# Kernel tuning notes

Hardware: AMD Instinct MI355X
Metric: run time of the kernel (lower is better)

Reference implementation:

```python
import jax, jax.numpy as jnp
import numpy as np

B, S, D, E = 4, 4096, 512, 8
H = 4 * D


def setup_inputs() -> dict:
    key = jax.random.key(0)
    ks = jax.random.split(key, 10)
    s_d = 1.0 / np.sqrt(D)
    s_h = 1.0 / np.sqrt(H)
    return {
        "x": jax.random.normal(ks[0], (B, S, D), jnp.float32),
        "Wr": jax.random.uniform(ks[1], (D, E), jnp.float32, -s_d, s_d),
        "br": jax.random.uniform(ks[2], (E,), jnp.float32, -s_d, s_d),
        "Wn": jax.random.uniform(ks[3], (D, E), jnp.float32, -s_d, s_d),
        "bn": jax.random.uniform(ks[4], (E,), jnp.float32, -s_d, s_d),
        "W1": jax.random.uniform(ks[5], (E, D, H), jnp.float32, -s_d, s_d),
        "b1": jax.random.uniform(ks[6], (E, H), jnp.float32, -s_d, s_d),
        "W2": jax.random.uniform(ks[7], (E, H, D), jnp.float32, -s_h, s_h),
        "b2": jax.random.uniform(ks[8], (E, D), jnp.float32, -s_h, s_h),
        "top_k": 2,
    }


def reference(x, Wr, br, Wn, bn, W1, b1, W2, b2, top_k):
    d = x.shape[-1]
    flat = x.reshape(-1, d)                      # [T, D]
    T = flat.shape[0]
    # --- NoisyTopkRouter ---
    logits = flat @ Wr + br                      # [T, E]
    noisy_lin = flat @ Wn + bn                   # [T, E]
    noise = jax.random.normal(jax.random.key(42), logits.shape, logits.dtype)
    noisy_logits = logits + noise * jax.nn.softplus(noisy_lin)
    topv, topi = jax.lax.top_k(noisy_logits, top_k)  # [T, K]
    sparse = jnp.full_like(noisy_logits, -jnp.inf)
    sparse = sparse.at[jnp.arange(T)[:, None], topi].set(topv)
    gate = jax.nn.softmax(sparse, axis=-1)       # zeros at non-topk (exp(-inf)=0)
    # --- expert compute + combine ---
    # gate is exactly 0 for non-selected experts, so dense per-expert compute
    # weighted by gate is math-identical to the masked gather/scatter loop.
    # Dropout(0.1) is identity in eval mode.
    out = jnp.zeros_like(flat)
    n_experts = W1.shape[0]
    for e in range(n_experts):
        h = jax.nn.relu(flat @ W1[e] + b1[e])    # [T, H]
        y = h @ W2[e] + b2[e]                    # [T, D]
        out = out + gate[:, e:e + 1] * y
    return out.reshape(x.shape)
```

## Files before the change

### kernel.cpp

```cpp
#include <hip/hip_runtime.h>
#include <hip/hip_bf16.h>
#include <stdint.h>
#include <math.h>

#define T_TOKENS 16384
#define DIM      512
#define NEXP     8
#define HID      2048

typedef __attribute__((ext_vector_type(8))) __bf16 bf16x8;
typedef __attribute__((ext_vector_type(16))) float f32x16;

__device__ __forceinline__ f32x16 mfma32(bf16x8 a, bf16x8 b, f32x16 c) {
  return __builtin_amdgcn_mfma_f32_32x32x16_bf16(a, b, c, 0, 0, 0);
}

__device__ __forceinline__ void glds16(const __bf16* g, __bf16* l) {
  __builtin_amdgcn_global_load_lds((const __attribute__((address_space(1))) void*)g,
                                   (__attribute__((address_space(3))) void*)l, 16, 0, 0);
}

#define WAITVM(n) asm volatile("s_waitcnt vmcnt(" #n ")" ::: "memory")
#define WAITLGKM0 asm volatile("s_waitcnt lgkmcnt(0)" ::: "memory")
#define SBAR      asm volatile("s_barrier" ::: "memory")
#define SCHEDB    __builtin_amdgcn_sched_barrier(0)
#define ADV3(v)   v = ((v) == 2) ? 0 : ((v) + 1)

__device__ __forceinline__ void threefry2x32(uint32_t k0, uint32_t k1,
                                             uint32_t x0, uint32_t x1,
                                             uint32_t* o0, uint32_t* o1) {
  uint32_t ks0 = k0, ks1 = k1, ks2 = k0 ^ k1 ^ 0x1BD11BDAu;
#define TF_ROT(v, d) (((v) << (d)) | ((v) >> (32 - (d))))
#define TF_ROUND(r) { x0 += x1; x1 = TF_ROT(x1, r); x1 ^= x0; }
  x0 += ks0; x1 += ks1;
  TF_ROUND(13) TF_ROUND(15) TF_ROUND(26) TF_ROUND(6)
  x0 += ks1; x1 += ks2 + 1u;
  TF_ROUND(17) TF_ROUND(29) TF_ROUND(16) TF_ROUND(24)
  x0 += ks2; x1 += ks0 + 2u;
  TF_ROUND(13) TF_ROUND(15) TF_ROUND(26) TF_ROUND(6)
  x0 += ks0; x1 += ks1 + 3u;
  TF_ROUND(17) TF_ROUND(29) TF_ROUND(16) TF_ROUND(24)
  x0 += ks1; x1 += ks2 + 4u;
  TF_ROUND(13) TF_ROUND(15) TF_ROUND(26) TF_ROUND(6)
  x0 += ks2; x1 += ks0 + 5u;
#undef TF_ROUND
#undef TF_ROT
  *o0 = x0; *o1 = x1;
}

__device__ __forceinline__ float erfinv_xla(float x) {
  float w = -log1pf(__fmul_rn(-x, x));
  float p;
  if (w < 5.0f) {
    w = __fadd_rn(w, -2.5f);
    p = 2.81022636e-08f;
    p = __fadd_rn(3.43273939e-07f, __fmul_rn(p, w));
    p = __fadd_rn(-3.5233877e-06f, __fmul_rn(p, w));
    p = __fadd_rn(-4.39150654e-06f, __fmul_rn(p, w));
    p = __fadd_rn(0.00021858087f, __fmul_rn(p, w));
    p = __fadd_rn(-0.00125372503f, __fmul_rn(p, w));
    p = __fadd_rn(-0.00417768164f, __fmul_rn(p, w));
    p = __fadd_rn(0.246640727f, __fmul_rn(p, w));
    p = __fadd_rn(1.50140941f, __fmul_rn(p, w));
  } else {
    w = __fadd_rn(sqrtf(w), -3.0f);
    p = -0.000200214257f;
    p = __fadd_rn(0.000100950558f, __fmul_rn(p, w));
    p = __fadd_rn(0.00134934322f, __fmul_rn(p, w));
    p = __fadd_rn(-0.00367342844f, __fmul_rn(p, w));
    p = __fadd_rn(0.00573950773f, __fmul_rn(p, w));
    p = __fadd_rn(-0.0076224613f, __fmul_rn(p, w));
    p = __fadd_rn(0.00943887047f, __fmul_rn(p, w));
    p = __fadd_rn(1.00167406f, __fmul_rn(p, w));
    p = __fadd_rn(2.83297682f, __fmul_rn(p, w));
  }
  return __fmul_rn(p, x);
}

__device__ __forceinline__ float jax_normal_at(uint32_t i) {
  uint32_t o0, o1;
  threefry2x32(0u, 42u, 0u, i, &o0, &o1);
  uint32_t bits = o0 ^ o1;
  float f = __fadd_rn(__uint_as_float((bits >> 9) | 0x3f800000u), -1.0f);
  const float lo = -0.99999994f;
  float u = fmaxf(lo, __fadd_rn(__fmul_rn(f, 2.0f), lo));
  return __fmul_rn(1.4142135623730951f, erfinv_xla(u));
}

__global__ __launch_bounds__(256) void prep_router(
    const float* __restrict__ x, const float* __restrict__ Wr, const float* __restrict__ br,
    const float* __restrict__ Wn, const float* __restrict__ bn,
    const float* __restrict__ W1, const float* __restrict__ W2,
    __bf16* __restrict__ W1p, __bf16* __restrict__ W2p,
    uint8_t* __restrict__ fillRow, uint32_t* __restrict__ ltok2,
    float* __restrict__ out) {
  __shared__ float Ls[64][68];
  __shared__ float WrS[4224], WnS[4224];
  __shared__ int lhist[8];
  const int tid = threadIdx.x;
  const int blk = blockIdx.x;

  {
    float4 z = {0.f, 0.f, 0.f, 0.f};
    ((float4*)out)[blk * 512 + tid] = z;
    ((float4*)out)[blk * 512 + 256 + tid] = z;
  }

  {
    const float* src; __bf16* dst; int R, C, e, rt, ct;
    if (blk < 2048) { e = blk >> 8; int rem = blk & 255; rt = rem >> 5; ct = rem & 31;
                      src = W1; dst = W1p; R = 512; C = 2048; }
    else            { int v2 = blk - 2048; e = v2 >> 8; int rem = v2 & 255; rt = rem >> 3; ct = rem & 7;
                      src = W2; dst = W2p; R = 2048; C = 512; }
    const float* sp = src + (size_t)e * R * C + (size_t)(rt * 64) * C + ct * 64;
    int row = tid >> 4, col = (tid & 15) * 4;
#pragma unroll
    for (int it = 0; it < 4; ++it)
      *(float4*)&Ls[it * 16 + row][col] = *(const float4*)(sp + (size_t)(it * 16 + row) * C + col);
    __syncthreads();
    int KO = R >> 3;
#pragma unroll
    for (int q = 0; q < 2; ++q) {
      int f = tid + q * 256;
      int lc = f & 31, kol = (f >> 5) & 7, ntl = f >> 8;
      bf16x8 vv;
#pragma unroll
      for (int j = 0; j < 8; ++j) vv[j] = (__bf16)Ls[kol * 8 + j][ntl * 32 + lc];
      size_t idx = ((size_t)(e * (C >> 5) + ct * 2 + ntl) * KO + rt * 8 + kol) * 256 + lc * 8;
      *(bf16x8*)(dst + idx) = vv;
    }
  }

  if (blk >= 256) return;

#pragma unroll
  for (int i = 0; i < 4; ++i) {
    int i4 = tid + i * 256;
    int d = i4 >> 1, eh = (i4 & 1) * 4;
    *(float4*)&WrS[d * 8 + (d >> 5) * 8 + eh] = ((const float4*)Wr)[i4];
    *(float4*)&WnS[d * 8 + (d >> 5) * 8 + eh] = ((const float4*)Wn)[i4];
  }
  if (tid < 8) lhist[tid] = 0;
  __syncthreads();

  const int w = tid >> 6, lane = tid & 63;
  const int tl = lane & 3, dq = lane >> 2;
  const int el = (lane >> 2) & 7;

  for (int p = 0; p < 4; ++p) {
    int t = blk * 64 + p * 16 + w * 4 + tl;

    const float* xp = x + (size_t)t * DIM + dq * 32;
    float xv[32];
#pragma unroll
    for (int i = 0; i < 8; ++i) {
      float4 f = *(const float4*)(xp + i * 4);
      xv[i * 4 + 0] = f.x; xv[i * 4 + 1] = f.y; xv[i * 4 + 2] = f.z; xv[i * 4 + 3] = f.w;
    }

    double accR[8], accN[8];
#pragma unroll
    for (int e2 = 0; e2 < 8; ++e2) { accR[e2] = 0.0; accN[e2] = 0.0; }
#pragma unroll
    for (int r = 0; r < 32; ++r) {
      int d = dq * 32 + r;
      const float* wr = &WrS[d * 8 + (d >> 5) * 8];
      const float* wn = &WnS[d * 8 + (d >> 5) * 8];
      double xd = (double)xv[r];
#pragma unroll
      for (int e2 = 0; e2 < 8; ++e2) {
        accR[e2] += xd * (double)wr[e2];
        accN[e2] += xd * (double)wn[e2];
      }
    }
#pragma unroll
    for (int m = 4; m <= 32; m <<= 1) {
#pragma unroll
      for (int e2 = 0; e2 < 8; ++e2) {
        accR[e2] += __shfl_xor(accR[e2], m);
        accN[e2] += __shfl_xor(accN[e2], m);
      }
    }

    double accRm = 0.0, accNm = 0.0;
#pragma unroll
    for (int e2 = 0; e2 < 8; ++e2) {
      double vR = __shfl(accR[e2], tl);
      double vN = __shfl(accN[e2], tl);
      if (e2 == el) { accRm = vR; accNm = vN; }
    }
    double noisy = -1.0e308;
    if (lane < 32) {
      double logit = accRm + (double)br[el];
      double nlin  = accNm + (double)bn[el];
      double noise = (double)jax_normal_at((uint32_t)t * 8u + (uint32_t)el);
      double sp = fmax(nlin, 0.0) + log1p(exp(-fabs(nlin)));
      noisy = logit + noise * sp;
    }
    double v[8];
#pragma unroll
    for (int e2 = 0; e2 < 8; ++e2) v[e2] = __shfl(noisy, tl + 4 * e2);

    if (lane < 4) {
      int i1 = 0; double v1 = v[0];
#pragma unroll
      for (int e2 = 1; e2 < 8; ++e2) if (v[e2] > v1) { v1 = v[e2]; i1 = e2; }
      int i2 = -1; double v2 = -1.0e308;
#pragma unroll
      for (int e2 = 0; e2 < 8; ++e2) if (e2 != i1 && v[e2] > v2) { v2 = v[e2]; i2 = e2; }
      double w2 = exp(v2 - v1);
      double s = 1.0 + w2;
      uint32_t q1 = (uint32_t)((1.0 / s) * 262143.0 + 0.5);
      uint32_t q2 = (uint32_t)((w2 / s) * 262143.0 + 0.5);
      int p1 = atomicAdd(&lhist[i1], 1);
      ltok2[(blk * 8 + i1) * 64 + p1] = (uint32_t)t | (q1 << 14);
      int p2 = atomicAdd(&lhist[i2], 1);
      ltok2[(blk * 8 + i2) * 64 + p2] = (uint32_t)t | (q2 << 14);
    }
  }
  __syncthreads();
  if (tid < 8) fillRow[blk * 8 + tid] = (uint8_t)lhist[tid];
}

__global__ __launch_bounds__(512) void expert_mfma(
    const float* __restrict__ x,
    const __bf16* __restrict__ W1p, const float* __restrict__ b1,
    const __bf16* __restrict__ W2p, const float* __restrict__ b2,
    const uint8_t* __restrict__ fillRow, const uint32_t* __restrict__ ltok2,
    float* __restrict__ out) {
  const int e = blockIdx.x & 7;
  const int tslot = blockIdx.x >> 3;

  __shared__ __bf16 Xs[64 * 512];
  __shared__ __bf16 Hs[64 * 256];
  __shared__ __bf16 Ring[8][3][1024];
  __shared__ int   toks[64];
  __shared__ float gates[64];
  __shared__ int   scanS[256];

  const int tid  = threadIdx.x;
  const int lane = tid & 63;
  const int w    = tid >> 6;
  const int hi   = lane >> 5;
  const int lm   = lane & 31;

  if (tid < 256) scanS[tid] = (int)fillRow[tid * 8 + e];
  __syncthreads();
  for (int d2 = 1; d2 < 256; d2 <<= 1) {
    int a = 0;
    if (tid < 256 && tid >= d2) a = scanS[tid - d2];
    __syncthreads();
    if (tid < 256 && tid >= d2) scanS[tid] += a;
    __syncthreads();
  }
  const int cnt = scanS[255];

  const __bf16* W1e = W1p + (size_t)e * (64 * 64 * 256);
  const __bf16* W2e = W2p + (size_t)e * (16 * 256 * 256);
  __bf16* ringW = &Ring[w][0][0];

  const float b2r0 = b2[e * DIM + (2 * w + 0) * 32 + lm];
  const float b2r1 = b2[e * DIM + (2 * w + 1) * 32 + lm];

  auto issueStage = [&](int g, int slot) {
    int hc = g >> 5, ss = g & 15;
    __bf16* dstL = ringW + slot * 1024;
    if (((g >> 4) & 1) == 0) {
      int nt = hc * 8 + w;
      const __bf16* srcp = W1e + ((size_t)(nt * 64 + ss * 4)) * 256 + lane * 8;
      glds16(srcp, dstL);
      glds16(srcp + 512, dstL + 512);
    } else {
      int ko2 = hc * 32 + ss * 2;
      glds16(W2e + ((size_t)((2 * w) * 256 + ko2)) * 256 + lane * 8, dstL);
      glds16(W2e + ((size_t)((2 * w + 1) * 256 + ko2)) * 256 + lane * 8, dstL + 512);
    }
  };

  for (int tile = tslot; tile * 64 < cnt; tile += 64) {
    int start = tile * 64;
    int nrow = min(64, cnt - start);

    issueStage(0, 0);
    issueStage(1, 1);

    SBAR;
    if (tid < 64) {
      int tk = 0; float g = 0.f;
      if (tid < nrow) {
        int rank = start + tid;
        int s = 0;
#pragma unroll
        for (int st = 128; st; st >>= 1) {
          int t2 = s + st;
          if (t2 < 256 && scanS[t2 - 1] <= rank) s = t2;
        }
        int ex = s ? scanS[s - 1] : 0;
        uint32_t en = ltok2[(s * 8 + e) * 64 + (rank - ex)];
        tk = (int)(en & 16383u);
        g = (float)(en >> 14) * (1.f / 262143.f);
      }
      toks[tid] = tk; gates[tid] = g;
    }
    WAITLGKM0; SBAR;

    {
      int tm = tid >> 3, seg = tid & 7;
      bool valid = tm < nrow;
      const float* xp = x + (size_t)(valid ? toks[tm] : toks[0]) * DIM + seg * 64;
#pragma unroll
      for (int s2 = 0; s2 < 8; ++s2) {
        bf16x8 v;
        if (valid) {
          float4 f0 = *(const float4*)(xp + s2 * 8);
          float4 f1 = *(const float4*)(xp + s2 * 8 + 4);
          v[0] = (__bf16)f0.x; v[1] = (__bf16)f0.y; v[2] = (__bf16)f0.z; v[3] = (__bf16)f0.w;
          v[4] = (__bf16)f1.x; v[5] = (__bf16)f1.y; v[6] = (__bf16)f1.z; v[7] = (__bf16)f1.w;
        } else {
#pragma unroll
          for (int j = 0; j < 8; ++j) v[j] = (__bf16)0.f;
        }
        int ko = seg * 8 + s2;
        *(bf16x8*)&Xs[((size_t)tm * 64 + (ko ^ (tm & 31))) * 8] = v;
      }
    }
    WAITLGKM0; SBAR;

    f32x16 acc200, acc201, acc210, acc211;
#pragma unroll
    for (int r = 0; r < 16; ++r) { acc200[r] = 0.f; acc201[r] = 0.f; acc210[r] = 0.f; acc211[r] = 0.f; }

    int cs = 0, is_ = 2;

    for (int hc = 0; hc < 8; ++hc) {
      float bias = b1[e * HID + (hc * 8 + w) * 32 + lm];
      f32x16 acc10, acc11;
#pragma unroll
      for (int r = 0; r < 16; ++r) { acc10[r] = 0.f; acc11[r] = 0.f; }

#pragma unroll
      for (int ss = 0; ss < 16; ++ss) {
        issueStage(hc * 32 + ss + 2, is_); ADV3(is_);
        WAITVM(4); SCHEDB;
        const __bf16* rb = ringW + cs * 1024; ADV3(cs);
#pragma unroll
        for (int kk = 0; kk < 2; ++kk) {
          int koX = (ss * 2 + kk) * 2 + hi;
          bf16x8 a0 = *(const bf16x8*)&Xs[((size_t)lm * 64 + (koX ^ lm)) * 8];
          bf16x8 a1 = *(const bf16x8*)&Xs[((size_t)(32 + lm) * 64 + (koX ^ lm)) * 8];
          bf16x8 b  = *(const bf16x8*)&rb[kk * 512 + hi * 256 + lm * 8];
          acc10 = mfma32(a0, b, acc10);
          acc11 = mfma32(a1, b, acc11);
        }
      }

#pragma unroll
      for (int m = 0; m < 2; ++m)
#pragma unroll
        for (int r = 0; r < 16; ++r) {
          int tok = (r & 3) + 8 * (r >> 2) + 4 * hi + 32 * m;
          float v = fmaxf((m ? acc11[r] : acc10[r]) + bias, 0.f);
          int koW = (w * 4 + (lm >> 3)) ^ (tok & 31);
          Hs[((size_t)tok * 32 + koW) * 8 + (lm & 7)] = (__bf16)v;
        }
      WAITLGKM0; SBAR;

#pragma unroll
      for (int ss = 0; ss < 16; ++ss) {
        if (hc < 7 || ss < 14) { issueStage(hc * 32 + 16 + ss + 2, is_); ADV3(is_); }
        if (hc < 7 || ss < 14) { WAITVM(4); }
        else if (ss == 14)     { WAITVM(2); }
        else                   { WAITVM(0); }
        SCHEDB;
        const __bf16* rb = ringW + cs * 1024; ADV3(cs);
        int koH = ss * 2 + hi;
        bf16x8 h0  = *(const bf16x8*)&Hs[((size_t)lm * 32 + (koH ^ lm)) * 8];
        bf16x8 h1  = *(const bf16x8*)&Hs[((size_t)(32 + lm) * 32 + (koH ^ lm)) * 8];
        bf16x8 b0  = *(const bf16x8*)&rb[hi * 256 + lm * 8];
        bf16x8 b1v = *(const bf16x8*)&rb[512 + hi * 256 + lm * 8];
        acc200 = mfma32(h0, b0, acc200);
        acc201 = mfma32(h1, b0, acc201);
        acc210 = mfma32(h0, b1v, acc210);
        acc211 = mfma32(h1, b1v, acc211);
      }
      SBAR;
    }

    {
      int d0 = (2 * w) * 32 + lm;
      int d1 = (2 * w + 1) * 32 + lm;
#pragma unroll
      for (int m = 0; m < 2; ++m)
#pragma unroll
        for (int r = 0; r < 16; ++r) {
          int row = (r & 3) + 8 * (r >> 2) + 4 * hi + 32 * m;
          int tk = toks[row];
          float gg = gates[row];
          float* op = out + (size_t)tk * DIM;
          atomicAdd(op + d0, gg * ((m ? acc201[r] : acc200[r]) + b2r0));
          atomicAdd(op + d1, gg * ((m ? acc211[r] : acc210[r]) + b2r1));
        }
    }
  }
}

extern "C" void kernel_launch(void* const* d_in, const int* in_sizes, int n_in,
                              void* d_out, int out_size, void* d_ws, size_t ws_size,
                              hipStream_t stream) {
  const float* x  = (const float*)d_in[0];
  const float* Wr = (const float*)d_in[1];
  const float* br = (const float*)d_in[2];
  const float* Wn = (const float*)d_in[3];
  const float* bn = (const float*)d_in[4];
  const float* W1 = (const float*)d_in[5];
  const float* b1 = (const float*)d_in[6];
  const float* W2 = (const float*)d_in[7];
  const float* b2 = (const float*)d_in[8];
  float* out = (float*)d_out;

  uint8_t* wsb = (uint8_t*)d_ws;
  uint8_t*  fillRow = wsb;
  uint32_t* ltok2   = (uint32_t*)(wsb + 2048);
  __bf16*   W1p     = (__bf16*)(wsb + 526336);
  __bf16*   W2p     = (__bf16*)(wsb + 526336 + 16777216);

  prep_router<<<4096, 256, 0, stream>>>(x, Wr, br, Wn, bn, W1, W2, W1p, W2p,
                                        fillRow, ltok2, out);
  expert_mfma<<<512, 512, 0, stream>>>(x, W1p, b1, W2p, b2, fillRow, ltok2, out);
}
```

Before: 521.3 us.

## Use 128-token tiles with register-prefetched weights instead of LDS weight ring

```diff
diff --git a/kernel.cpp b/kernel.cpp
--- a/kernel.cpp
+++ b/kernel.cpp
@@ -15,16 +15,8 @@
   return __builtin_amdgcn_mfma_f32_32x32x16_bf16(a, b, c, 0, 0, 0);
 }
 
-__device__ __forceinline__ void glds16(const __bf16* g, __bf16* l) {
-  __builtin_amdgcn_global_load_lds((const __attribute__((address_space(1))) void*)g,
-                                   (__attribute__((address_space(3))) void*)l, 16, 0, 0);
-}
-
-#define WAITVM(n) asm volatile("s_waitcnt vmcnt(" #n ")" ::: "memory")
 #define WAITLGKM0 asm volatile("s_waitcnt lgkmcnt(0)" ::: "memory")
 #define SBAR      asm volatile("s_barrier" ::: "memory")
-#define SCHEDB    __builtin_amdgcn_sched_barrier(0)
-#define ADV3(v)   v = ((v) == 2) ? 0 : ((v) + 1)
 
 __device__ __forceinline__ void threefry2x32(uint32_t k0, uint32_t k1,
                                              uint32_t x0, uint32_t x1,
@@ -222,7 +214,7 @@
   if (tid < 8) fillRow[blk * 8 + tid] = (uint8_t)lhist[tid];
 }
 
-__global__ __launch_bounds__(512) void expert_mfma(
+__global__ __launch_bounds__(512, 2) void expert_mfma(
     const float* __restrict__ x,
     const __bf16* __restrict__ W1p, const float* __restrict__ b1,
     const __bf16* __restrict__ W2p, const float* __restrict__ b2,
@@ -231,12 +223,11 @@
   const int e = blockIdx.x & 7;
   const int tslot = blockIdx.x >> 3;
 
-  __shared__ __bf16 Xs[64 * 512];
-  __shared__ __bf16 Hs[64 * 256];
-  __shared__ __bf16 Ring[8][3][1024];
-  __shared__ int   toks[64];
-  __shared__ float gates[64];
-  __shared__ int   scanS[256];
+  __shared__ __bf16 Xs[128 * 64 * 8];
+  __shared__ __bf16 Hs[128 * 16 * 8];
+  int*   scanS = (int*)Hs;
+  int*   toksT = (int*)Hs + 256;
+  float* gateT = (float*)((int*)Hs + 384);
 
   const int tid  = threadIdx.x;
   const int lane = tid & 63;
@@ -244,48 +235,35 @@
   const int hi   = lane >> 5;
   const int lm   = lane & 31;
 
-  if (tid < 256) scanS[tid] = (int)fillRow[tid * 8 + e];
-  __syncthreads();
-  for (int d2 = 1; d2 < 256; d2 <<= 1) {
-    int a = 0;
-    if (tid < 256 && tid >= d2) a = scanS[tid - d2];
-    __syncthreads();
-    if (tid < 256 && tid >= d2) scanS[tid] += a;
-    __syncthreads();
-  }
-  const int cnt = scanS[255];
+  int cnt = 0;
+#pragma unroll
+  for (int j = 0; j < 4; ++j) cnt += (int)fillRow[(lane * 4 + j) * 8 + e];
+#pragma unroll
+  for (int m = 1; m < 64; m <<= 1) cnt += __shfl_xor(cnt, m);
 
   const __bf16* W1e = W1p + (size_t)e * (64 * 64 * 256);
   const __bf16* W2e = W2p + (size_t)e * (16 * 256 * 256);
-  __bf16* ringW = &Ring[w][0][0];
-
-  const float b2r0 = b2[e * DIM + (2 * w + 0) * 32 + lm];
-  const float b2r1 = b2[e * DIM + (2 * w + 1) * 32 + lm];
-
-  auto issueStage = [&](int g, int slot) {
-    int hc = g >> 5, ss = g & 15;
-    __bf16* dstL = ringW + slot * 1024;
-    if (((g >> 4) & 1) == 0) {
-      int nt = hc * 8 + w;
-      const __bf16* srcp = W1e + ((size_t)(nt * 64 + ss * 4)) * 256 + lane * 8;
-      glds16(srcp, dstL);
-      glds16(srcp + 512, dstL + 512);
-    } else {
-      int ko2 = hc * 32 + ss * 2;
-      glds16(W2e + ((size_t)((2 * w) * 256 + ko2)) * 256 + lane * 8, dstL);
-      glds16(W2e + ((size_t)((2 * w + 1) * 256 + ko2)) * 256 + lane * 8, dstL + 512);
-    }
-  };
-
-  for (int tile = tslot; tile * 64 < cnt; tile += 64) {
-    int start = tile * 64;
-    int nrow = min(64, cnt - start);
-
-    issueStage(0, 0);
-    issueStage(1, 1);
-
-    SBAR;
-    if (tid < 64) {
+
+  const float b2r0 = b2[e * DIM + w * 64 + lm];
+  const float b2r1 = b2[e * DIM + w * 64 + 32 + lm];
+
+  for (int tile = tslot; tile * 128 < cnt; tile += 32) {
+    int start = tile * 128;
+    int nrow = min(128, cnt - start);
+
+    __syncthreads();
+
+    if (tid < 256) scanS[tid] = (int)fillRow[tid * 8 + e];
+    __syncthreads();
+    for (int d2 = 1; d2 < 256; d2 <<= 1) {
+      int a = 0;
+      if (tid < 256 && tid >= d2) a = scanS[tid - d2];
+      __syncthreads();
+      if (tid < 256 && tid >= d2) scanS[tid] += a;
+      __syncthreads();
+    }
+
+    if (tid < 128) {
       int tk = 0; float g = 0.f;
       if (tid < nrow) {
         int rank = start + tid;
@@ -300,16 +278,19 @@
         tk = (int)(en & 16383u);
         g = (float)(en >> 14) * (1.f / 262143.f);
       }
-      toks[tid] = tk; gates[tid] = g;
-    }
-    WAITLGKM0; SBAR;
+      toksT[tid] = tk; gateT[tid] = g;
+    }
+    __syncthreads();
+
+    const int   t0 = toksT[lane], t1 = toksT[64 + lane];
+    const float g0 = gateT[lane], g1 = gateT[64 + lane];
 
     {
-      int tm = tid >> 3, seg = tid & 7;
+      int tm = tid >> 2, q = tid & 3;
       bool valid = tm < nrow;
-      const float* xp = x + (size_t)(valid ? toks[tm] : toks[0]) * DIM + seg * 64;
-#pragma unroll
-      for (int s2 = 0; s2 < 8; ++s2) {
+      const float* xp = x + (size_t)(valid ? toksT[tm] : toksT[0]) * DIM + q * 128;
+#pragma unroll
+      for (int s2 = 0; s2 < 16; ++s2) {
         bf16x8 v;
         if (valid) {
           float4 f0 = *(const float4*)(xp + s2 * 8);
@@ -320,85 +301,100 @@
 #pragma unroll
           for (int j = 0; j < 8; ++j) v[j] = (__bf16)0.f;
         }
-        int ko = seg * 8 + s2;
+        int ko = q * 16 + s2;
         *(bf16x8*)&Xs[((size_t)tm * 64 + (ko ^ (tm & 31))) * 8] = v;
       }
     }
-    WAITLGKM0; SBAR;
-
-    f32x16 acc200, acc201, acc210, acc211;
-#pragma unroll
-    for (int r = 0; r < 16; ++r) { acc200[r] = 0.f; acc201[r] = 0.f; acc210[r] = 0.f; acc211[r] = 0.f; }
-
-    int cs = 0, is_ = 2;
-
-    for (int hc = 0; hc < 8; ++hc) {
-      float bias = b1[e * HID + (hc * 8 + w) * 32 + lm];
-      f32x16 acc10, acc11;
-#pragma unroll
-      for (int r = 0; r < 16; ++r) { acc10[r] = 0.f; acc11[r] = 0.f; }
-
-#pragma unroll
-      for (int ss = 0; ss < 16; ++ss) {
-        issueStage(hc * 32 + ss + 2, is_); ADV3(is_);
-        WAITVM(4); SCHEDB;
-        const __bf16* rb = ringW + cs * 1024; ADV3(cs);
-#pragma unroll
-        for (int kk = 0; kk < 2; ++kk) {
-          int koX = (ss * 2 + kk) * 2 + hi;
-          bf16x8 a0 = *(const bf16x8*)&Xs[((size_t)lm * 64 + (koX ^ lm)) * 8];
-          bf16x8 a1 = *(const bf16x8*)&Xs[((size_t)(32 + lm) * 64 + (koX ^ lm)) * 8];
-          bf16x8 b  = *(const bf16x8*)&rb[kk * 512 + hi * 256 + lm * 8];
-          acc10 = mfma32(a0, b, acc10);
-          acc11 = mfma32(a1, b, acc11);
-        }
-      }
-
-#pragma unroll
-      for (int m = 0; m < 2; ++m)
+    __syncthreads();
+
+    f32x16 acc2[2][4];
+#pragma unroll
+    for (int t = 0; t < 2; ++t)
+#pragma unroll
+      for (int g = 0; g < 4; ++g)
+#pragma unroll
+        for (int r = 0; r < 16; ++r) acc2[t][g][r] = 0.f;
+
+    for (int c = 0; c < 8; ++c) {
+      const __bf16* w1l = W1e + ((size_t)((c * 8 + w) * 64)) * 256 + lm * 8;
+      f32x16 acc1[4];
+#pragma unroll
+      for (int g = 0; g < 4; ++g)
+#pragma unroll
+        for (int r = 0; r < 16; ++r) acc1[g][r] = 0.f;
+
+      bf16x8 wcur = *(const bf16x8*)(w1l + (size_t)hi * 256);
+#pragma unroll
+      for (int ks = 0; ks < 32; ++ks) {
+        bf16x8 wnxt;
+        if (ks < 31) wnxt = *(const bf16x8*)(w1l + (size_t)((ks + 1) * 2 + hi) * 256);
+        int swz = (ks * 2 + hi) ^ lm;
+#pragma unroll
+        for (int g = 0; g < 4; ++g) {
+          bf16x8 a = *(const bf16x8*)&Xs[((size_t)(g * 32 + lm) * 64 + swz) * 8];
+          acc1[g] = mfma32(a, wcur, acc1[g]);
+        }
+        wcur = wnxt;
+      }
+
+      float bias = b1[e * HID + (c * 8 + w) * 32 + lm];
+      __bf16 hreg[4][16];
+#pragma unroll
+      for (int g = 0; g < 4; ++g)
+#pragma unroll
+        for (int r = 0; r < 16; ++r)
+          hreg[g][r] = (__bf16)fmaxf(acc1[g][r] + bias, 0.f);
+
+#pragma unroll
+      for (int half = 0; half < 2; ++half) {
+        if ((w >> 2) == half) {
+          int koB = (w & 3) * 4 + (lm >> 3);
+#pragma unroll
+          for (int g = 0; g < 4; ++g)
+#pragma unroll
+            for (int r = 0; r < 16; ++r) {
+              int tok = (r & 3) + 8 * (r >> 2) + 4 * hi + 32 * g;
+              Hs[((size_t)tok * 16 + (koB ^ (tok & 15))) * 8 + (lm & 7)] = hreg[g][r];
+            }
+        }
+        WAITLGKM0; SBAR;
+
+        const __bf16* w2l = W2e + ((size_t)((2 * w) * 256 + c * 32 + half * 16)) * 256 + lm * 8;
+        bf16x8 c0 = *(const bf16x8*)(w2l + (size_t)hi * 256);
+        bf16x8 c1 = *(const bf16x8*)(w2l + 65536 + (size_t)hi * 256);
+#pragma unroll
+        for (int ks2 = 0; ks2 < 8; ++ks2) {
+          bf16x8 n0, n1;
+          if (ks2 < 7) {
+            n0 = *(const bf16x8*)(w2l + (size_t)((ks2 + 1) * 2 + hi) * 256);
+            n1 = *(const bf16x8*)(w2l + 65536 + (size_t)((ks2 + 1) * 2 + hi) * 256);
+          }
+          int koH = ks2 * 2 + hi;
+          int swzH = koH ^ (lm & 15);
+#pragma unroll
+          for (int g = 0; g < 4; ++g) {
+            bf16x8 ha = *(const bf16x8*)&Hs[((size_t)(g * 32 + lm) * 16 + swzH) * 8];
+            acc2[0][g] = mfma32(ha, c0, acc2[0][g]);
+            acc2[1][g] = mfma32(ha, c1, acc2[1][g]);
+          }
+          c0 = n0; c1 = n1;
+        }
+        SBAR;
+      }
+    }
+
+#pragma unroll
+    for (int t = 0; t < 2; ++t) {
+      int d = w * 64 + t * 32 + lm;
+      float b2v = t ? b2r1 : b2r0;
+#pragma unroll
+      for (int g = 0; g < 4; ++g)
 #pragma unroll
         for (int r = 0; r < 16; ++r) {
-          int tok = (r & 3) + 8 * (r >> 2) + 4 * hi + 32 * m;
-          float v = fmaxf((m ? acc11[r] : acc10[r]) + bias, 0.f);
-          int koW = (w * 4 + (lm >> 3)) ^ (tok & 31);
-          Hs[((size_t)tok * 32 + koW) * 8 + (lm & 7)] = (__bf16)v;
-        }
-      WAITLGKM0; SBAR;
-
-#pragma unroll
-      for (int ss = 0; ss < 16; ++ss) {
-        if (hc < 7 || ss < 14) { issueStage(hc * 32 + 16 + ss + 2, is_); ADV3(is_); }
-        if (hc < 7 || ss < 14) { WAITVM(4); }
-        else if (ss == 14)     { WAITVM(2); }
-        else                   { WAITVM(0); }
-        SCHEDB;
-        const __bf16* rb = ringW + cs * 1024; ADV3(cs);
-        int koH = ss * 2 + hi;
-        bf16x8 h0  = *(const bf16x8*)&Hs[((size_t)lm * 32 + (koH ^ lm)) * 8];
-        bf16x8 h1  = *(const bf16x8*)&Hs[((size_t)(32 + lm) * 32 + (koH ^ lm)) * 8];
-        bf16x8 b0  = *(const bf16x8*)&rb[hi * 256 + lm * 8];
-        bf16x8 b1v = *(const bf16x8*)&rb[512 + hi * 256 + lm * 8];
-        acc200 = mfma32(h0, b0, acc200);
-        acc201 = mfma32(h1, b0, acc201);
-        acc210 = mfma32(h0, b1v, acc210);
-        acc211 = mfma32(h1, b1v, acc211);
-      }
-      SBAR;
-    }
-
-    {
-      int d0 = (2 * w) * 32 + lm;
-      int d1 = (2 * w + 1) * 32 + lm;
-#pragma unroll
-      for (int m = 0; m < 2; ++m)
-#pragma unroll
-        for (int r = 0; r < 16; ++r) {
-          int row = (r & 3) + 8 * (r >> 2) + 4 * hi + 32 * m;
-          int tk = toks[row];
-          float gg = gates[row];
-          float* op = out + (size_t)tk * DIM;
-          atomicAdd(op + d0, gg * ((m ? acc201[r] : acc200[r]) + b2r0));
-          atomicAdd(op + d1, gg * ((m ? acc211[r] : acc210[r]) + b2r1));
+          int row = (r & 3) + 8 * (r >> 2) + 4 * hi + 32 * g;
+          int   tokv = __shfl(g < 2 ? t0 : t1, row & 63);
+          float gv   = __shfl(g < 2 ? g0 : g1, row & 63);
+          atomicAdd(out + (size_t)tokv * DIM + d, gv * (acc2[t][g][r] + b2v));
         }
     }
   }
@@ -426,5 +422,5 @@
 
   prep_router<<<4096, 256, 0, stream>>>(x, Wr, br, Wn, bn, W1, W2, W1p, W2p,
                                         fillRow, ltok2, out);
-  expert_mfma<<<512, 512, 0, stream>>>(x, W1p, b1, W2p, b2, fillRow, ltok2, out);
-}
+  expert_mfma<<<256, 512, 0, stream>>>(x, W1p, b1, W2p, b2, fillRow, ltok2, out);
+}
```

After: 911.6 us. 74.9% more time.
